# Performance work log

Hardware: AMD Instinct MI355X
Metric: run time of the kernel (lower is better)

Reference implementation:

```python
import jax, jax.numpy as jnp
import numpy as np

N_NODES = 100000
N_EDGES = 1600000
HIDDEN = 64
EPS = 1e-5


def setup_inputs() -> dict:
    key = jax.random.key(0)
    ks = jax.random.split(key, 12)
    h = HIDDEN
    inp = {
        'x': jax.random.normal(ks[0], (N_NODES, h), dtype=jnp.float32),
        'edge_index': jax.random.randint(ks[1], (2, N_EDGES), 0, N_NODES, dtype=jnp.int32),
        'message': jax.random.normal(ks[2], (N_EDGES, h), dtype=jnp.float32),
        # node_mlp: Linear(2h->h), BN(h), ReLU, Dropout(identity), Linear(h->h), BN(h), ReLU
        'W1': jax.random.normal(ks[3], (2 * h, h), dtype=jnp.float32) / np.sqrt(2.0 * h),
        'b1': jnp.zeros((h,), jnp.float32),
        'g1': jnp.ones((h,), jnp.float32),
        'be1': jnp.zeros((h,), jnp.float32),
        'W2': jax.random.normal(ks[4], (h, h), dtype=jnp.float32) / np.sqrt(h),
        'b2': jnp.zeros((h,), jnp.float32),
        'g2': jnp.ones((h,), jnp.float32),
        'be2': jnp.zeros((h,), jnp.float32),
        # attention_mlp: Linear(h->1), Sigmoid
        'Wa': jax.random.normal(ks[5], (h, 1), dtype=jnp.float32) / np.sqrt(h),
        'ba': jnp.zeros((1,), jnp.float32),
    }
    return inp


def _scatter_max(msg, idx, n):
    # torch_scatter scatter(..., reduce='max') fills segments with no edges with 0
    agg = jax.ops.segment_max(msg, idx, num_segments=n)  # [N, H], -inf where empty
    cnt = jax.ops.segment_sum(jnp.ones((idx.shape[0],), msg.dtype), idx, num_segments=n)
    return jnp.where(cnt[:, None] > 0, agg, jnp.zeros((), msg.dtype))


def _batchnorm(x, gamma, beta):
    # training-mode BatchNorm1d: batch mean / biased variance
    mu = jnp.mean(x, axis=0)
    var = jnp.mean((x - mu) ** 2, axis=0)
    return (x - mu) * jax.lax.rsqrt(var + EPS) * gamma + beta


def reference(x, edge_index, message, W1, b1, g1, be1, W2, b2, g2, be2, Wa, ba):
    n = x.shape[0]
    row, col = edge_index[0], edge_index[1]
    fwd = _scatter_max(message, col, n)   # [N, H]
    bwd = _scatter_max(message, row, n)   # [N, H]
    out = jnp.concatenate([fwd, bwd], axis=1)          # [N, 2H]
    h1 = jax.nn.relu(_batchnorm(out @ W1 + b1, g1, be1))  # dropout = identity (eval)
    h2 = jax.nn.relu(_batchnorm(h1 @ W2 + b2, g2, be2))   # [N, H]
    att = jax.nn.sigmoid(h2 @ Wa + ba).reshape(-1)          # [N]
    return (h2, att)
```

## Files before the change

kernel.cpp:

```cpp
#include <hip/hip_runtime.h>
#include <hip/hip_bf16.h>
#include <cstdint>
#include <cstddef>

#define HDIM 64
#define EPS 1e-5f
#define BN 128
#define BSH 7
#define NXCD 8
#define BCAPX 2560
#define CURPAD 16
#define SENTE 128u
static const unsigned SENT = 0x007FFFFFu;

typedef short bf16x8 __attribute__((ext_vector_type(8)));
typedef float f32x4  __attribute__((ext_vector_type(4)));
typedef float f4v    __attribute__((ext_vector_type(4)));
typedef unsigned u2v __attribute__((ext_vector_type(2)));

__device__ __forceinline__ unsigned bf16rn(float f) {
    unsigned u = __float_as_uint(f);
    return (u + 0x7FFFu + ((u >> 16) & 1u)) >> 16;
}

__device__ __forceinline__ unsigned flipf(float f) {
    unsigned u = __float_as_uint(f);
    return u ^ (((unsigned)((int)u >> 31)) | 0x80000000u);
}

__device__ __forceinline__ float unflip(unsigned u) {
    if (u == SENT) return 0.0f;
    unsigned b = (u & 0x80000000u) ? (u & 0x7FFFFFFFu) : ~u;
    return __uint_as_float(b);
}

__global__ __launch_bounds__(256) void bucket_fill_kernel(
    const int* __restrict__ ei, unsigned* __restrict__ bcur,
    unsigned* __restrict__ entries, int E, int nblk) {
    int e = blockIdx.x * 256 + threadIdx.x;
    if (e >= E) return;
    unsigned xcd;
    asm volatile("s_getreg_b32 %0, hwreg(HW_REG_XCC_ID)" : "=s"(xcd));
    xcd &= (NXCD - 1);
    int row = ei[e];
    int col = ei[(size_t)E + e];
    unsigned cell1 = (unsigned)(col >> BSH) * NXCD + xcd;
    unsigned cell2 = (unsigned)(nblk + (row >> BSH)) * NXCD + xcd;
    unsigned p1 = atomicAdd(&bcur[(size_t)cell1 * CURPAD], 1u);
    unsigned p2 = atomicAdd(&bcur[(size_t)cell2 * CURPAD], 1u);
    if (p1 < BCAPX)
        entries[(size_t)cell1 * BCAPX + p1] = ((unsigned)e << 8) | (unsigned)(col & (BN - 1));
    if (p2 < BCAPX)
        entries[(size_t)cell2 * BCAPX + p2] = ((unsigned)e << 8) | (unsigned)(row & (BN - 1));
}

__global__ __launch_bounds__(256) void binned_max_kernel(
    const float* __restrict__ msg, const unsigned* __restrict__ bcur,
    const unsigned* __restrict__ entries,
    unsigned short* __restrict__ fwdB, unsigned short* __restrict__ bwdB,
    int N, int nblk) {
    __shared__ __align__(16) unsigned acc[(BN + 1) * HDIM];
    int tid = threadIdx.x;
    int wave = tid >> 6, lane = tid & 63;
    int b = blockIdx.x;

    {
        uint4 sv; sv.x = SENT; sv.y = SENT; sv.z = SENT; sv.w = SENT;
        uint4* p = (uint4*)acc;
        for (int i = tid; i < (BN + 1) * HDIM / 4; i += 256) p[i] = sv;
    }
    __syncthreads();

    unsigned accBase = (unsigned)(size_t)&acc[0];
    unsigned laneOff = accBase + ((unsigned)lane << 2);

    for (int rr = 0; rr < 2; ++rr) {
        int r = wave + rr * 4;
        unsigned cnt = bcur[((size_t)b * NXCD + r) * CURPAD];
        if (cnt > BCAPX) cnt = BCAPX;
        const unsigned* rb = entries + ((size_t)b * NXCD + r) * BCAPX;
        for (unsigned c0 = 0; c0 < cnt; c0 += 64) {
            unsigned myent = (c0 + (unsigned)lane < cnt) ? rb[c0 + lane] : SENTE;
            unsigned rem = cnt - c0;
#pragma unroll
            for (int b16 = 0; b16 < 4; ++b16) {
                if ((unsigned)(b16 * 16) >= rem) break;
                float v[16];
#pragma unroll
                for (int k = 0; k < 16; ++k) {
                    unsigned ent = __shfl(myent, b16 * 16 + k);
                    v[k] = __builtin_nontemporal_load(&msg[(size_t)(ent >> 8) * HDIM + lane]);
                }
#pragma unroll
                for (int k = 0; k < 16; ++k) {
                    unsigned ent = __shfl(myent, b16 * 16 + k);
                    unsigned addr = laneOff + ((ent & 255u) << 8);
                    asm volatile("ds_max_u32 %0, %1" :: "v"(addr), "v"(flipf(v[k])));
                }
            }
        }
    }
    asm volatile("" ::: "memory");
    __syncthreads();

    bool fwd = (b < nblk);
    int node0 = (fwd ? b : b - nblk) * BN;
    unsigned short* dst = fwd ? fwdB : bwdB;
    for (int i = tid; i < BN * (HDIM / 4); i += 256) {
        int rrow = i >> 4, c4 = (i & 15) * 4;
        int node = node0 + rrow;
        if (node >= N) continue;
        uint4 a = *(const uint4*)&acc[rrow * HDIM + c4];
        float v0 = unflip(a.x), v1 = unflip(a.y);
        float v2 = unflip(a.z), v3 = unflip(a.w);
        u2v o;
        o.x = bf16rn(v0) | (bf16rn(v1) << 16);
        o.y = bf16rn(v2) | (bf16rn(v3) << 16);
        *(u2v*)(dst + (size_t)node * HDIM + c4) = o;
    }
}


__global__ __launch_bounds__(256) void prep_w_kernel(
    const float* __restrict__ W1, const float* __restrict__ W2,
    unsigned short* __restrict__ W1T, unsigned short* __restrict__ W2T) {
    int t = blockIdx.x * 256 + threadIdx.x;
    if (t < 128 * 64) {
        int k = t >> 6, o = t & 63;
        W1T[o * 128 + k] = (unsigned short)bf16rn(W1[t]);
    } else {
        int t2 = t - 128 * 64;
        if (t2 < 64 * 64) {
            int k = t2 >> 6, o = t2 & 63;
            W2T[o * 64 + k] = (unsigned short)bf16rn(W2[t2]);
        }
    }
}

__global__ __launch_bounds__(256) void gemm1_mfma_kernel(
    const unsigned short* __restrict__ fwdB, const unsigned short* __restrict__ bwdB,
    const unsigned short* __restrict__ W1T, const float* __restrict__ b1,
    float* __restrict__ y1, float* __restrict__ sum1, float* __restrict__ sq1, int N) {
    __shared__ float wsum[4][64], wsq[4][64];
    int tid = threadIdx.x;
    int wave = tid >> 6, lane = tid & 63;
    int lrow = lane & 15, kseg = lane >> 4;
    int rbase = blockIdx.x * 64 + wave * 16;

    bf16x8 bfr[4][4];
#pragma unroll
    for (int nt = 0; nt < 4; ++nt)
#pragma unroll
        for (int kb = 0; kb < 4; ++kb)
            bfr[nt][kb] = *(const bf16x8*)(W1T + (size_t)(nt * 16 + lrow) * 128 + kb * 32 + kseg * 8);

    int r = rbase + lrow;
    bool ok = (r < N);
    size_t ro = (size_t)(ok ? r : 0) * HDIM;
    bf16x8 z = {};
    bf16x8 afr[4];
    afr[0] = *(const bf16x8*)(fwdB + ro + kseg * 8);
    afr[1] = *(const bf16x8*)(fwdB + ro + 32 + kseg * 8);
    afr[2] = *(const bf16x8*)(bwdB + ro + kseg * 8);
    afr[3] = *(const bf16x8*)(bwdB + ro + 32 + kseg * 8);
    if (!ok) { afr[0] = z; afr[1] = z; afr[2] = z; afr[3] = z; }

    f32x4 acc[4] = {};
#pragma unroll
    for (int kb = 0; kb < 4; ++kb)
#pragma unroll
        for (int nt = 0; nt < 4; ++nt)
            acc[nt] = __builtin_amdgcn_mfma_f32_16x16x32_bf16(afr[kb], bfr[nt][kb], acc[nt], 0, 0, 0);

#pragma unroll
    for (int nt = 0; nt < 4; ++nt) {
        int col = nt * 16 + lrow;
        float bias = b1[col];
        float s = 0.f, q = 0.f;
#pragma unroll
        for (int rr = 0; rr < 4; ++rr) {
            int rowi = rbase + kseg * 4 + rr;
            if (rowi < N) {
                float v = acc[nt][rr] + bias;
                y1[(size_t)rowi * HDIM + col] = v;
                s += v; q += v * v;
            }
        }
        s += __shfl_xor(s, 16); s += __shfl_xor(s, 32);
        q += __shfl_xor(q, 16); q += __shfl_xor(q, 32);
        if (kseg == 0) { wsum[wave][col] = s; wsq[wave][col] = q; }
    }
    __syncthreads();
    if (tid < 64) {
        float S = wsum[0][tid] + wsum[1][tid] + wsum[2][tid] + wsum[3][tid];
        float Q = wsq[0][tid] + wsq[1][tid] + wsq[2][tid] + wsq[3][tid];
        atomicAdd(&sum1[tid], S);
        atomicAdd(&sq1[tid], Q);
    }
}

__global__ __launch_bounds__(256) void gemm2_mfma_kernel(
    const float* __restrict__ y1, const float* __restrict__ sum1, const float* __restrict__ sq1,
    const float* __restrict__ g1, const float* __restrict__ be1,
    const unsigned short* __restrict__ W2T, const float* __restrict__ b2,
    float* __restrict__ y2, float* __restrict__ sum2, float* __restrict__ sq2, int N) {
    __shared__ float sc[64], sh[64];
    __shared__ float wsum[4][64], wsq[4][64];
    int tid = threadIdx.x;
    if (tid < 64) {
        float invN = 1.0f / (float)N;
        float mu = sum1[tid] * invN;
        float var = sq1[tid] * invN - mu * mu;
        float rs = rsqrtf(var + EPS);
        float s = rs * g1[tid];
        sc[tid] = s;
        sh[tid] = be1[tid] - mu * s;
    }
    __syncthreads();
    int wave = tid >> 6, lane = tid & 63;
    int lrow = lane & 15, kseg = lane >> 4;
    int rbase = blockIdx.x * 64 + wave * 16;

    bf16x8 bfr[4][2];
#pragma unroll
    for (int nt = 0; nt < 4; ++nt)
#pragma unroll
        for (int kb = 0; kb < 2; ++kb)
            bfr[nt][kb] = *(const bf16x8*)(W2T + (size_t)(nt * 16 + lrow) * 64 + kb * 32 + kseg * 8);

    int r = rbase + lrow;
    size_t ro = (size_t)((r < N) ? r : 0) * HDIM;
    bf16x8 afr[2];
#pragma unroll
    for (int kb = 0; kb < 2; ++kb) {
        const f4v* yp = (const f4v*)(y1 + ro + kb * 32 + kseg * 8);
        f4v u0 = yp[0], u1 = yp[1];
        int k0 = kb * 32 + kseg * 8;
        bf16x8 a;
#pragma unroll
        for (int j = 0; j < 4; ++j) {
            float h0 = fmaxf(fmaf(u0[j], sc[k0 + j], sh[k0 + j]), 0.f);
            float h1 = fmaxf(fmaf(u1[j], sc[k0 + 4 + j], sh[k0 + 4 + j]), 0.f);
            a[j] = (short)bf16rn(h0);
            a[4 + j] = (short)bf16rn(h1);
        }
        afr[kb] = a;
    }

    f32x4 acc[4] = {};
#pragma unroll
    for (int kb = 0; kb < 2; ++kb)
#pragma unroll
        for (int nt = 0; nt < 4; ++nt)
            acc[nt] = __builtin_amdgcn_mfma_f32_16x16x32_bf16(afr[kb], bfr[nt][kb], acc[nt], 0, 0, 0);

#pragma unroll
    for (int nt = 0; nt < 4; ++nt) {
        int col = nt * 16 + lrow;
        float bias = b2[col];
        float s = 0.f, q = 0.f;
#pragma unroll
        for (int rr = 0; rr < 4; ++rr) {
            int rowi = rbase + kseg * 4 + rr;
            if (rowi < N) {
                float v = acc[nt][rr] + bias;
                y2[(size_t)rowi * HDIM + col] = v;
                s += v; q += v * v;
            }
        }
        s += __shfl_xor(s, 16); s += __shfl_xor(s, 32);
        q += __shfl_xor(q, 16); q += __shfl_xor(q, 32);
        if (kseg == 0) { wsum[wave][col] = s; wsq[wave][col] = q; }
    }
    __syncthreads();
    if (tid < 64) {
        float S = wsum[0][tid] + wsum[1][tid] + wsum[2][tid] + wsum[3][tid];
        float Q = wsq[0][tid] + wsq[1][tid] + wsq[2][tid] + wsq[3][tid];
        atomicAdd(&sum2[tid], S);
        atomicAdd(&sq2[tid], Q);
    }
}

__global__ __launch_bounds__(256) void final_kernel(
    const float* __restrict__ y2, const float* __restrict__ sum2, const float* __restrict__ sq2,
    const float* __restrict__ g2, const float* __restrict__ be2,
    const float* __restrict__ Wa, const float* __restrict__ ba,
    float* __restrict__ out_h2, float* __restrict__ out_att, int N) {
    __shared__ float sc[HDIM], sh[HDIM], wa[HDIM];
    __shared__ float bav;
    if (threadIdx.x < HDIM) {
        int c = threadIdx.x;
        float invN = 1.0f / (float)N;
        float mu = sum2[c] * invN;
        float var = sq2[c] * invN - mu * mu;
        float rstd = rsqrtf(var + EPS);
        float s = rstd * g2[c];
        sc[c] = s;
        sh[c] = be2[c] - mu * s;
        wa[c] = Wa[c];
    }
    if (threadIdx.x == 0) bav = ba[0];
    __syncthreads();
    int n = blockIdx.x * 256 + threadIdx.x;
    if (n >= N) return;

    const f4v* p = (const f4v*)&y2[(size_t)n * HDIM];
    f4v* dst = (f4v*)&out_h2[(size_t)n * HDIM];
    float att = bav;
#pragma unroll 1
    for (int kk = 0; kk < 16; ++kk) {
        f4v u = p[kk];
        f4v hv;
#pragma unroll
        for (int j = 0; j < 4; ++j) {
            int k = kk * 4 + j;
            float h = fmaxf(fmaf(u[j], sc[k], sh[k]), 0.0f);
            hv[j] = h;
            att = fmaf(h, wa[k], att);
        }
        dst[kk] = hv;
    }
    out_att[n] = 1.0f / (1.0f + expf(-att));
}

extern "C" void kernel_launch(void* const* d_in, const int* in_sizes, int n_in,
                              void* d_out, int out_size, void* d_ws, size_t ws_size,
                              hipStream_t stream) {
    const int*   ei   = (const int*)d_in[1];
    const float* msg  = (const float*)d_in[2];
    const float* W1   = (const float*)d_in[3];
    const float* b1   = (const float*)d_in[4];
    const float* g1   = (const float*)d_in[5];
    const float* be1  = (const float*)d_in[6];
    const float* W2   = (const float*)d_in[7];
    const float* b2   = (const float*)d_in[8];
    const float* g2   = (const float*)d_in[9];
    const float* be2  = (const float*)d_in[10];
    const float* Wa   = (const float*)d_in[11];
    const float* ba   = (const float*)d_in[12];

    const int N = in_sizes[0] / HDIM;
    const int E = in_sizes[1] / 2;
    const int nblk = (N + BN - 1) / BN;

    unsigned short* fwdB = (unsigned short*)d_ws;
    unsigned short* bwdB = fwdB + (size_t)N * HDIM;
    unsigned short* W1T  = bwdB + (size_t)N * HDIM;
    unsigned short* W2T  = W1T + 8192;
    float*    stats      = (float*)(W2T + 4096);
    unsigned* bcur       = (unsigned*)(stats + 256);
    unsigned* entries    = bcur + (size_t)2 * nblk * NXCD * CURPAD;
    float*    y1         = (float*)d_out;
    float*    y2         = (float*)d_ws;
    float*    out_att    = (float*)d_out + (size_t)N * HDIM;

    hipMemsetAsync(stats, 0, 256 * sizeof(float)
                             + (size_t)2 * nblk * NXCD * CURPAD * sizeof(unsigned), stream);
    prep_w_kernel<<<48, 256, 0, stream>>>(W1, W2, W1T, W2T);

    int eblocks = (E + 255) / 256;
    bucket_fill_kernel<<<eblocks, 256, 0, stream>>>(ei, bcur, entries, E, nblk);
    binned_max_kernel<<<2 * nblk, 256, 0, stream>>>(msg, bcur, entries, fwdB, bwdB, N, nblk);

    int G = (N + 63) / 64;
    gemm1_mfma_kernel<<<G, 256, 0, stream>>>(fwdB, bwdB, W1T, b1, y1,
                                             stats, stats + 64, N);
    gemm2_mfma_kernel<<<G, 256, 0, stream>>>(y1, stats, stats + 64, g1, be1,
                                             W2T, b2, y2, stats + 128, stats + 192, N);
    final_kernel<<<(N + 255) / 256, 256, 0, stream>>>(y2, stats + 128, stats + 192,
                                                      g2, be2, Wa, ba,
                                                      (float*)d_out, out_att, N);
}
```

Measured before the change: 429.9 us.

## Pre-convert messages to order-preserving bf16 keys before binned max gather

Adds a streaming pass that converts each fp32 message to a bf16 key whose unsigned order matches float order. The binned max kernel then gathers 2-byte keys instead of 4-byte floats and feeds them straight into ds_max_u32 with a zero sentinel. The weight prep and bucket fill are merged into the same launch. This halves the bytes per random gather but adds a full read plus a half-size write of the message tensor.

```diff
diff --git a/kernel.cpp b/kernel.cpp
--- a/kernel.cpp
+++ b/kernel.cpp
@@ -11,51 +11,83 @@
 #define BCAPX 2560
 #define CURPAD 16
 #define SENTE 128u
-static const unsigned SENT = 0x007FFFFFu;
 
 typedef short bf16x8 __attribute__((ext_vector_type(8)));
 typedef float f32x4  __attribute__((ext_vector_type(4)));
 typedef float f4v    __attribute__((ext_vector_type(4)));
 typedef unsigned u2v __attribute__((ext_vector_type(2)));
+typedef unsigned u4v __attribute__((ext_vector_type(4)));
 
 __device__ __forceinline__ unsigned bf16rn(float f) {
     unsigned u = __float_as_uint(f);
     return (u + 0x7FFFu + ((u >> 16) & 1u)) >> 16;
 }
 
-__device__ __forceinline__ unsigned flipf(float f) {
-    unsigned u = __float_as_uint(f);
-    return u ^ (((unsigned)((int)u >> 31)) | 0x80000000u);
-}
-
-__device__ __forceinline__ float unflip(unsigned u) {
-    if (u == SENT) return 0.0f;
-    unsigned b = (u & 0x80000000u) ? (u & 0x7FFFFFFFu) : ~u;
-    return __uint_as_float(b);
-}
-
-__global__ __launch_bounds__(256) void bucket_fill_kernel(
+__device__ __forceinline__ unsigned flipbf(float f) {
+    unsigned h = bf16rn(f);
+    return (h & 0x8000u) ? (~h & 0xFFFFu) : (h | 0x8000u);
+}
+
+__device__ __forceinline__ unsigned unflipkey(unsigned key) {
+    if (key == 0u) return 0u;
+    unsigned k = key >> 16;
+    return (k & 0x8000u) ? (k & 0x7FFFu) : (~k & 0xFFFFu);
+}
+
+__global__ __launch_bounds__(256) void prep_kernel(
+    const float* __restrict__ msg, unsigned short* __restrict__ msgB,
     const int* __restrict__ ei, unsigned* __restrict__ bcur,
-    unsigned* __restrict__ entries, int E, int nblk) {
-    int e = blockIdx.x * 256 + threadIdx.x;
-    if (e >= E) return;
-    unsigned xcd;
-    asm volatile("s_getreg_b32 %0, hwreg(HW_REG_XCC_ID)" : "=s"(xcd));
-    xcd &= (NXCD - 1);
-    int row = ei[e];
-    int col = ei[(size_t)E + e];
-    unsigned cell1 = (unsigned)(col >> BSH) * NXCD + xcd;
-    unsigned cell2 = (unsigned)(nblk + (row >> BSH)) * NXCD + xcd;
-    unsigned p1 = atomicAdd(&bcur[(size_t)cell1 * CURPAD], 1u);
-    unsigned p2 = atomicAdd(&bcur[(size_t)cell2 * CURPAD], 1u);
-    if (p1 < BCAPX)
-        entries[(size_t)cell1 * BCAPX + p1] = ((unsigned)e << 8) | (unsigned)(col & (BN - 1));
-    if (p2 < BCAPX)
-        entries[(size_t)cell2 * BCAPX + p2] = ((unsigned)e << 8) | (unsigned)(row & (BN - 1));
+    unsigned* __restrict__ entries,
+    const float* __restrict__ W1, const float* __restrict__ W2,
+    unsigned short* __restrict__ W1T, unsigned short* __restrict__ W2T,
+    int E, int nblk, int cblocks, int eblocks) {
+    int blk = blockIdx.x;
+    if (blk < cblocks) {
+        size_t i = ((size_t)blk * 256 + threadIdx.x) * 8;
+        size_t total = (size_t)E * HDIM;
+        if (i < total) {
+            f4v a = __builtin_nontemporal_load((const f4v*)&msg[i]);
+            f4v b = __builtin_nontemporal_load((const f4v*)&msg[i + 4]);
+            u4v o;
+            o.x = flipbf(a.x) | (flipbf(a.y) << 16);
+            o.y = flipbf(a.z) | (flipbf(a.w) << 16);
+            o.z = flipbf(b.x) | (flipbf(b.y) << 16);
+            o.w = flipbf(b.z) | (flipbf(b.w) << 16);
+            __builtin_nontemporal_store(o, (u4v*)&msgB[i]);
+        }
+    } else if (blk < cblocks + eblocks) {
+        int e = (blk - cblocks) * 256 + threadIdx.x;
+        if (e >= E) return;
+        unsigned xcd;
+        asm volatile("s_getreg_b32 %0, hwreg(HW_REG_XCC_ID)" : "=s"(xcd));
+        xcd &= (NXCD - 1);
+        int row = ei[e];
+        int col = ei[(size_t)E + e];
+        unsigned cell1 = (unsigned)(col >> BSH) * NXCD + xcd;
+        unsigned cell2 = (unsigned)(nblk + (row >> BSH)) * NXCD + xcd;
+        unsigned p1 = atomicAdd(&bcur[(size_t)cell1 * CURPAD], 1u);
+        unsigned p2 = atomicAdd(&bcur[(size_t)cell2 * CURPAD], 1u);
+        if (p1 < BCAPX)
+            entries[(size_t)cell1 * BCAPX + p1] = ((unsigned)e << 8) | (unsigned)(col & (BN - 1));
+        if (p2 < BCAPX)
+            entries[(size_t)cell2 * BCAPX + p2] = ((unsigned)e << 8) | (unsigned)(row & (BN - 1));
+    } else {
+        int t = (blk - cblocks - eblocks) * 256 + threadIdx.x;
+        if (t < 128 * 64) {
+            int k = t >> 6, o = t & 63;
+            W1T[o * 128 + k] = (unsigned short)bf16rn(W1[t]);
+        } else {
+            int t2 = t - 128 * 64;
+            if (t2 < 64 * 64) {
+                int k = t2 >> 6, o = t2 & 63;
+                W2T[o * 64 + k] = (unsigned short)bf16rn(W2[t2]);
+            }
+        }
+    }
 }
 
 __global__ __launch_bounds__(256) void binned_max_kernel(
-    const float* __restrict__ msg, const unsigned* __restrict__ bcur,
+    const unsigned short* __restrict__ msgB, const unsigned* __restrict__ bcur,
     const unsigned* __restrict__ entries,
     unsigned short* __restrict__ fwdB, unsigned short* __restrict__ bwdB,
     int N, int nblk) {
@@ -65,9 +97,9 @@
     int b = blockIdx.x;
 
     {
-        uint4 sv; sv.x = SENT; sv.y = SENT; sv.z = SENT; sv.w = SENT;
-        uint4* p = (uint4*)acc;
-        for (int i = tid; i < (BN + 1) * HDIM / 4; i += 256) p[i] = sv;
+        u4v z = {};
+        u4v* p = (u4v*)acc;
+        for (int i = tid; i < (BN + 1) * HDIM / 4; i += 256) p[i] = z;
     }
     __syncthreads();
 
@@ -85,17 +117,18 @@
 #pragma unroll
             for (int b16 = 0; b16 < 4; ++b16) {
                 if ((unsigned)(b16 * 16) >= rem) break;
-                float v[16];
+                unsigned short v[16];
 #pragma unroll
                 for (int k = 0; k < 16; ++k) {
                     unsigned ent = __shfl(myent, b16 * 16 + k);
-                    v[k] = __builtin_nontemporal_load(&msg[(size_t)(ent >> 8) * HDIM + lane]);
+                    v[k] = __builtin_nontemporal_load(&msgB[(size_t)(ent >> 8) * HDIM + lane]);
                 }
 #pragma unroll
                 for (int k = 0; k < 16; ++k) {
                     unsigned ent = __shfl(myent, b16 * 16 + k);
                     unsigned addr = laneOff + ((ent & 255u) << 8);
-                    asm volatile("ds_max_u32 %0, %1" :: "v"(addr), "v"(flipf(v[k])));
+                    unsigned key = ((unsigned)v[k]) << 16;
+                    asm volatile("ds_max_u32 %0, %1" :: "v"(addr), "v"(key));
                 }
             }
         }
@@ -111,31 +144,13 @@
         int node = node0 + rrow;
         if (node >= N) continue;
         uint4 a = *(const uint4*)&acc[rrow * HDIM + c4];
-        float v0 = unflip(a.x), v1 = unflip(a.y);
-        float v2 = unflip(a.z), v3 = unflip(a.w);
         u2v o;
-        o.x = bf16rn(v0) | (bf16rn(v1) << 16);
-        o.y = bf16rn(v2) | (bf16rn(v3) << 16);
+        o.x = unflipkey(a.x) | (unflipkey(a.y) << 16);
+        o.y = unflipkey(a.z) | (unflipkey(a.w) << 16);
         *(u2v*)(dst + (size_t)node * HDIM + c4) = o;
     }
 }
 
-
-__global__ __launch_bounds__(256) void prep_w_kernel(
-    const float* __restrict__ W1, const float* __restrict__ W2,
-    unsigned short* __restrict__ W1T, unsigned short* __restrict__ W2T) {
-    int t = blockIdx.x * 256 + threadIdx.x;
-    if (t < 128 * 64) {
-        int k = t >> 6, o = t & 63;
-        W1T[o * 128 + k] = (unsigned short)bf16rn(W1[t]);
-    } else {
-        int t2 = t - 128 * 64;
-        if (t2 < 64 * 64) {
-            int k = t2 >> 6, o = t2 & 63;
-            W2T[o * 64 + k] = (unsigned short)bf16rn(W2[t2]);
-        }
-    }
-}
 
 __global__ __launch_bounds__(256) void gemm1_mfma_kernel(
     const unsigned short* __restrict__ fwdB, const unsigned short* __restrict__ bwdB,
@@ -350,17 +365,21 @@
     float*    stats      = (float*)(W2T + 4096);
     unsigned* bcur       = (unsigned*)(stats + 256);
     unsigned* entries    = bcur + (size_t)2 * nblk * NXCD * CURPAD;
+    unsigned short* msgB = (unsigned short*)(entries + (size_t)2 * nblk * NXCD * BCAPX);
     float*    y1         = (float*)d_out;
     float*    y2         = (float*)d_ws;
     float*    out_att    = (float*)d_out + (size_t)N * HDIM;
 
     hipMemsetAsync(stats, 0, 256 * sizeof(float)
                              + (size_t)2 * nblk * NXCD * CURPAD * sizeof(unsigned), stream);
-    prep_w_kernel<<<48, 256, 0, stream>>>(W1, W2, W1T, W2T);
-
+
+    int cblocks = (int)(((size_t)E * HDIM / 8 + 255) / 256);
     int eblocks = (E + 255) / 256;
-    bucket_fill_kernel<<<eblocks, 256, 0, stream>>>(ei, bcur, entries, E, nblk);
-    binned_max_kernel<<<2 * nblk, 256, 0, stream>>>(msg, bcur, entries, fwdB, bwdB, N, nblk);
+    int wblocks = 48;
+    prep_kernel<<<cblocks + eblocks + wblocks, 256, 0, stream>>>(
+        msg, msgB, ei, bcur, entries, W1, W2, W1T, W2T, E, nblk, cblocks, eblocks);
+
+    binned_max_kernel<<<2 * nblk, 256, 0, stream>>>(msgB, bcur, entries, fwdB, bwdB, N, nblk);
 
     int G = (N + 63) / 64;
     gemm1_mfma_kernel<<<G, 256, 0, stream>>>(fwdB, bwdB, W1T, b1, y1,
```

Result: slower. 468.7 us (+9.0%).

## Software-pipeline message gathers in binned max and fuse weight prep into bucket fill

Applied to the files above, without the earlier changes.

The binned max loop now issues the next 16 message row loads, and the next 64-entry index chunk, before running the LDS max atomics on the current batch. This double buffering is meant to hide global load latency behind the ds_max work. Separately, the weight transpose and bf16 conversion kernel is folded into extra blocks of the bucket fill kernel, which removes one kernel launch. The cost is more registers per thread in the max kernel, which may lower occupancy.

```diff
diff --git a/kernel.cpp b/kernel.cpp
--- a/kernel.cpp
+++ b/kernel.cpp
@@ -17,6 +17,7 @@
 typedef float f32x4  __attribute__((ext_vector_type(4)));
 typedef float f4v    __attribute__((ext_vector_type(4)));
 typedef unsigned u2v __attribute__((ext_vector_type(2)));
+typedef unsigned u4v __attribute__((ext_vector_type(4)));
 
 __device__ __forceinline__ unsigned bf16rn(float f) {
     unsigned u = __float_as_uint(f);
@@ -34,10 +35,28 @@
     return __uint_as_float(b);
 }
 
-__global__ __launch_bounds__(256) void bucket_fill_kernel(
+__global__ __launch_bounds__(256) void fill_kernel(
     const int* __restrict__ ei, unsigned* __restrict__ bcur,
-    unsigned* __restrict__ entries, int E, int nblk) {
-    int e = blockIdx.x * 256 + threadIdx.x;
+    unsigned* __restrict__ entries,
+    const float* __restrict__ W1, const float* __restrict__ W2,
+    unsigned short* __restrict__ W1T, unsigned short* __restrict__ W2T,
+    int E, int nblk, int eblocks) {
+    int blk = blockIdx.x;
+    if (blk >= eblocks) {
+        int t = (blk - eblocks) * 256 + threadIdx.x;
+        if (t < 128 * 64) {
+            int k = t >> 6, o = t & 63;
+            W1T[o * 128 + k] = (unsigned short)bf16rn(W1[t]);
+        } else {
+            int t2 = t - 128 * 64;
+            if (t2 < 64 * 64) {
+                int k = t2 >> 6, o = t2 & 63;
+                W2T[o * 64 + k] = (unsigned short)bf16rn(W2[t2]);
+            }
+        }
+        return;
+    }
+    int e = blk * 256 + threadIdx.x;
     if (e >= E) return;
     unsigned xcd;
     asm volatile("s_getreg_b32 %0, hwreg(HW_REG_XCC_ID)" : "=s"(xcd));
@@ -65,8 +84,8 @@
     int b = blockIdx.x;
 
     {
-        uint4 sv; sv.x = SENT; sv.y = SENT; sv.z = SENT; sv.w = SENT;
-        uint4* p = (uint4*)acc;
+        u4v sv; sv.x = SENT; sv.y = SENT; sv.z = SENT; sv.w = SENT;
+        u4v* p = (u4v*)acc;
         for (int i = tid; i < (BN + 1) * HDIM / 4; i += 256) p[i] = sv;
     }
     __syncthreads();
@@ -78,26 +97,50 @@
         int r = wave + rr * 4;
         unsigned cnt = bcur[((size_t)b * NXCD + r) * CURPAD];
         if (cnt > BCAPX) cnt = BCAPX;
+        if (cnt == 0) continue;
         const unsigned* rb = entries + ((size_t)b * NXCD + r) * BCAPX;
+
+        unsigned cur = ((unsigned)lane < cnt) ? rb[lane] : SENTE;
+        float v[16];
+#pragma unroll
+        for (int k = 0; k < 16; ++k) {
+            unsigned ent = __shfl(cur, k);
+            v[k] = __builtin_nontemporal_load(&msg[(size_t)(ent >> 8) * HDIM + lane]);
+        }
+
         for (unsigned c0 = 0; c0 < cnt; c0 += 64) {
-            unsigned myent = (c0 + (unsigned)lane < cnt) ? rb[c0 + lane] : SENTE;
             unsigned rem = cnt - c0;
+            unsigned nxt = SENTE;
+            bool havenxt = (c0 + 64 < cnt);
+            if (havenxt)
+                nxt = (c0 + 64 + (unsigned)lane < cnt) ? rb[c0 + 64 + lane] : SENTE;
 #pragma unroll
             for (int b16 = 0; b16 < 4; ++b16) {
                 if ((unsigned)(b16 * 16) >= rem) break;
-                float v[16];
+                bool hn = (c0 + (unsigned)((b16 + 1) * 16) < cnt);
+                float vn[16];
+                if (hn) {
+                    unsigned src = (b16 < 3) ? cur : nxt;
+                    int kb = (b16 < 3) ? (b16 + 1) * 16 : 0;
+#pragma unroll
+                    for (int k = 0; k < 16; ++k) {
+                        unsigned ent = __shfl(src, kb + k);
+                        vn[k] = __builtin_nontemporal_load(
+                            &msg[(size_t)(ent >> 8) * HDIM + lane]);
+                    }
+                }
 #pragma unroll
                 for (int k = 0; k < 16; ++k) {
-                    unsigned ent = __shfl(myent, b16 * 16 + k);
-                    v[k] = __builtin_nontemporal_load(&msg[(size_t)(ent >> 8) * HDIM + lane]);
-                }
-#pragma unroll
-                for (int k = 0; k < 16; ++k) {
-                    unsigned ent = __shfl(myent, b16 * 16 + k);
+                    unsigned ent = __shfl(cur, b16 * 16 + k);
                     unsigned addr = laneOff + ((ent & 255u) << 8);
                     asm volatile("ds_max_u32 %0, %1" :: "v"(addr), "v"(flipf(v[k])));
                 }
+                if (hn) {
+#pragma unroll
+                    for (int k = 0; k < 16; ++k) v[k] = vn[k];
+                }
             }
+            cur = nxt;
         }
     }
     asm volatile("" ::: "memory");
@@ -120,22 +163,6 @@
     }
 }
 
-
-__global__ __launch_bounds__(256) void prep_w_kernel(
-    const float* __restrict__ W1, const float* __restrict__ W2,
-    unsigned short* __restrict__ W1T, unsigned short* __restrict__ W2T) {
-    int t = blockIdx.x * 256 + threadIdx.x;
-    if (t < 128 * 64) {
-        int k = t >> 6, o = t & 63;
-        W1T[o * 128 + k] = (unsigned short)bf16rn(W1[t]);
-    } else {
-        int t2 = t - 128 * 64;
-        if (t2 < 64 * 64) {
-            int k = t2 >> 6, o = t2 & 63;
-            W2T[o * 64 + k] = (unsigned short)bf16rn(W2[t2]);
-        }
-    }
-}
 
 __global__ __launch_bounds__(256) void gemm1_mfma_kernel(
     const unsigned short* __restrict__ fwdB, const unsigned short* __restrict__ bwdB,
@@ -356,10 +383,11 @@
 
     hipMemsetAsync(stats, 0, 256 * sizeof(float)
                              + (size_t)2 * nblk * NXCD * CURPAD * sizeof(unsigned), stream);
-    prep_w_kernel<<<48, 256, 0, stream>>>(W1, W2, W1T, W2T);
 
     int eblocks = (E + 255) / 256;
-    bucket_fill_kernel<<<eblocks, 256, 0, stream>>>(ei, bcur, entries, E, nblk);
+    fill_kernel<<<eblocks + 48, 256, 0, stream>>>(ei, bcur, entries, W1, W2,
+                                                  W1T, W2T, E, nblk, eblocks);
+
     binned_max_kernel<<<2 * nblk, 256, 0, stream>>>(msg, bcur, entries, fwdB, bwdB, N, nblk);
 
     int G = (N + 63) / 64;
```

Result: slower. 439.3 us (+2.2%).
